# Performance work log

Hardware: AMD Instinct MI355X
Metric: run time of the kernel (lower is better)

## Reference

```python
import jax, jax.numpy as jnp
import numpy as np

EPS = 216.0 / 24389.0
KAPPA = 24389.0 / 27.0
WP = jnp.array([0.95047, 1.0, 1.08883], dtype=jnp.float32)  # D65 white point
M_RGB2XYZ = jnp.array([[0.4124564, 0.3575761, 0.1804375],
                       [0.2126729, 0.7151522, 0.0721750],
                       [0.0193339, 0.1191920, 0.9503041]], dtype=jnp.float32)
M_XYZ2RGB = jnp.array([[3.2404542, -1.5371385, -0.4985314],
                       [-0.9692660, 1.8760108, 0.0415560],
                       [0.0556434, -0.2040259, 1.0572252]], dtype=jnp.float32)
GRID = 8          # cv2.createCLAHE tileGridSize=(8,8)
CLIP_LIMIT = 2.0  # cv2.createCLAHE clipLimit=2.0
NBINS = 256


def _srgb_to_linear(c):
    return jnp.where(c <= 0.04045, c / 12.92, ((c + 0.055) / 1.055) ** 2.4)


def _linear_to_srgb(c):
    c = jnp.maximum(c, 0.0)
    return jnp.where(c <= 0.0031308, c * 12.92, 1.055 * c ** (1.0 / 2.4) - 0.055)


def _rgb_to_lab(rgb):  # rgb [...,3] in [0,1]
    xyz = _srgb_to_linear(rgb) @ M_RGB2XYZ.T / WP
    f = jnp.where(xyz > EPS, jnp.cbrt(xyz), (KAPPA * xyz + 16.0) / 116.0)
    L = 116.0 * f[..., 1] - 16.0
    a = 500.0 * (f[..., 0] - f[..., 1])
    b = 200.0 * (f[..., 1] - f[..., 2])
    return L, a, b


def _lab_to_rgb(L, a, b):
    fy = (L + 16.0) / 116.0
    fx = fy + a / 500.0
    fz = fy - b / 200.0
    def finv(f):
        f3 = f ** 3
        return jnp.where(f3 > EPS, f3, (116.0 * f - 16.0) / KAPPA)
    xyz = jnp.stack([finv(fx), finv(fy), finv(fz)], axis=-1) * WP
    return jnp.clip(_linear_to_srgb(xyz @ M_XYZ2RGB.T), 0.0, 1.0)


def _quantize_L(L):  # cv2.normalize(..., 0, 255, NORM_MINMAX) per image + uint8 cast
    lmin = L.min(axis=(1, 2), keepdims=True)
    lmax = L.max(axis=(1, 2), keepdims=True)
    l255 = (L - lmin) / (lmax - lmin + 1e-6) * 255.0
    return jnp.clip(jnp.round(l255), 0, 255).astype(jnp.int32)


def _equalize_hist(l_int):  # cv2.equalizeHist per image, [N,H,W] int32 -> float levels
    N, H, W = l_int.shape
    seg = (jnp.arange(N, dtype=jnp.int32)[:, None, None] * NBINS + l_int).reshape(-1)
    hist = jax.ops.segment_sum(jnp.ones(seg.shape, jnp.float32), seg,
                               num_segments=N * NBINS).reshape(N, NBINS)
    lut = jnp.round(jnp.cumsum(hist, axis=1) * (255.0 / (H * W)))  # [N,256]
    return jnp.take_along_axis(lut, l_int.reshape(N, H * W), axis=1).reshape(N, H, W)


def _clahe(l_int):  # tiled clipped histogram equalization + bilinear LUT blend
    N, H, W = l_int.shape
    th, tw = H // GRID, W // GRID
    area = th * tw
    ty = jnp.arange(H, dtype=jnp.int32) // th
    tx = jnp.arange(W, dtype=jnp.int32) // tw
    tile = ty[:, None] * GRID + tx[None, :]                      # [H,W] tile id
    seg = ((jnp.arange(N, dtype=jnp.int32)[:, None, None] * (GRID * GRID) + tile)
           * NBINS + l_int).reshape(-1)
    hist = jax.ops.segment_sum(jnp.ones(seg.shape, jnp.float32), seg,
                               num_segments=N * GRID * GRID * NBINS
                               ).reshape(N, GRID, GRID, NBINS)
    limit = max(CLIP_LIMIT * area / NBINS, 1.0)                  # = 32 for 64x64 tiles
    clipped = jnp.minimum(hist, limit)
    excess = (hist - clipped).sum(axis=-1, keepdims=True)
    luts = jnp.round(jnp.cumsum(clipped + excess / NBINS, axis=-1) * (255.0 / area))
    # bilinear interpolation between the 4 neighbouring tile LUTs (border-clamped)
    cy = jnp.clip((jnp.arange(H, dtype=jnp.float32) + 0.5) / th - 0.5, 0.0, GRID - 1.0)
    cx = jnp.clip((jnp.arange(W, dtype=jnp.float32) + 0.5) / tw - 0.5, 0.0, GRID - 1.0)
    y0 = jnp.clip(jnp.floor(cy).astype(jnp.int32), 0, GRID - 2); y1 = y0 + 1
    x0 = jnp.clip(jnp.floor(cx).astype(jnp.int32), 0, GRID - 2); x1 = x0 + 1
    wy = (cy - y0)[:, None]
    wx = (cx - x0)[None, :]
    def per_image(lut, v):  # lut [GRID,GRID,256], v [H,W]
        v00 = lut[y0[:, None], x0[None, :], v]
        v01 = lut[y0[:, None], x1[None, :], v]
        v10 = lut[y1[:, None], x0[None, :], v]
        v11 = lut[y1[:, None], x1[None, :], v]
        top = v00 * (1.0 - wx) + v01 * wx
        bot = v10 * (1.0 - wx) + v11 * wx
        return top * (1.0 - wy) + bot * wy
    return jax.vmap(per_image)(luts, l_int)


def setup_inputs() -> dict:
    key = jax.random.key(0)
    x = jax.random.uniform(key, (16, 3, 512, 512), dtype=jnp.float32)
    return {"x": x}


def reference(x):
    rgb = jnp.transpose(x, (0, 2, 3, 1))          # NCHW -> NHWC
    L, a, b = _rgb_to_lab(rgb)
    l_int = _quantize_L(L)
    def recon(l255):
        out = _lab_to_rgb(l255 * (100.0 / 255.0), a, b)
        return jnp.transpose(out, (0, 3, 1, 2)) * 255.0  # uint8-valued like original
    return recon(_equalize_hist(l_int)), recon(_clahe(l_int))
```

## Files before the change

### kernel.cpp

```cpp
#include <hip/hip_runtime.h>

#define NIMG 16
#define HH 512
#define WW 512
#define HW (HH * WW)
#define NHW (NIMG * HW)
#define TILE 64
#define TILE_AREA (TILE * TILE)

#define EPSV ((float)(216.0 / 24389.0))
#define KAPV ((float)(24389.0 / 27.0))


__device__ __forceinline__ float pow24(float t) {
    float l   = __builtin_amdgcn_logf(t);
    float r   = __builtin_amdgcn_exp2f(l);
    float dl  = (t - r) * __builtin_amdgcn_rcpf(r) * 1.4426950408889634f;
    float ehi = 2.4f * l;
    float elo = __builtin_fmaf(2.4f, l, -ehi) + 2.4f * dl;
    float p   = __builtin_amdgcn_exp2f(ehi);
    return __builtin_fmaf(p * 0.6931471805599453f, elo, p);
}

__device__ __forceinline__ float cbrt_p(float v) {
    float l  = __builtin_amdgcn_logf(v);
    float t  = __builtin_amdgcn_exp2f(l * (1.0f / 3.0f));
    float t2 = t * t;
    float num = __builtin_fmaf(-t2, t, v);
    return __builtin_fmaf(num, __builtin_amdgcn_rcpf(3.0f * t2), t);
}

__device__ __forceinline__ float srgb2lin_p(float c) {
    float lin = c / 12.92f;
    float t   = (c + 0.055f) / 1.055f;
    return (c <= 0.04045f) ? lin : pow24(t);
}

__device__ __forceinline__ float fwd_p(float v) {
    return (v > EPSV) ? cbrt_p(v) : (KAPV * v + 16.0f) / 116.0f;
}

__device__ __forceinline__ float lin2srgb_f(float c) {
    c = fmaxf(c, 0.0f);
    float lo = c * 12.92f;
    float p  = __builtin_amdgcn_exp2f(__builtin_amdgcn_logf(c) * (float)(1.0 / 2.4));
    float hi = 1.055f * p - 0.055f;
    float r  = (c <= 0.0031308f) ? lo : hi;
    return fminf(fmaxf(r, 0.0f), 1.0f);
}

__device__ __forceinline__ float finv_f(float f) {
    float f3 = f * f * f;
    return (f3 > EPSV) ? f3 : (116.0f * f - 16.0f) * (float)(27.0 / 24389.0);
}

__device__ __forceinline__ void lab2rgb255_f(float L, float a, float b,
                                             float* R, float* G, float* B) {
    float fy = (L + 16.0f) * (float)(1.0 / 116.0);
    float fx = fy + a * (float)(1.0 / 500.0);
    float fz = fy - b * (float)(1.0 / 200.0);
    float X = finv_f(fx) * 0.95047f;
    float Y = finv_f(fy);
    float Z = finv_f(fz) * 1.08883f;
    *R = lin2srgb_f((float)3.2404542 * X + (float)-1.5371385 * Y + (float)-0.4985314 * Z) * 255.0f;
    *G = lin2srgb_f((float)-0.969266 * X + (float)1.8760108  * Y + (float)0.041556   * Z) * 255.0f;
    *B = lin2srgb_f((float)0.0556434 * X + (float)-0.2040259 * Y + (float)1.0572252  * Z) * 255.0f;
}

__device__ __forceinline__ unsigned f2o(float f) {
    unsigned b = __float_as_uint(f);
    return (b & 0x80000000u) ? ~b : (b | 0x80000000u);
}
__device__ __forceinline__ float o2f(unsigned o) {
    return __uint_as_float((o & 0x80000000u) ? (o ^ 0x80000000u) : ~o);
}


__global__ void k_init(unsigned* mm) {
    int t = blockIdx.x * 256 + threadIdx.x;
    if (t < NIMG * 64)
        mm[t] = ((t & 63) < 32) ? 0xFFFFFFFFu : 0u;
}

__global__ void k_lab(const float* __restrict__ x, float* __restrict__ out,
                      unsigned* __restrict__ mm) {
    int n = blockIdx.y;
    const float* img = x + (size_t)n * 3 * HW;
    float* o = out + (size_t)n * 3 * HW;
    int base = blockIdx.x * 2048;
    float mn = 1e30f, mx = -1e30f;
    for (int i = 0; i < 8; i++) {
        int p = base + i * 256 + threadIdx.x;
        float rl = srgb2lin_p(img[p]);
        float gl = srgb2lin_p(img[HW + p]);
        float bl = srgb2lin_p(img[2 * HW + p]);
        float X = ((float)0.4124564 * rl + (float)0.3575761 * gl + (float)0.1804375 * bl) / (float)0.95047;
        float Y = ((float)0.2126729 * rl + (float)0.7151522 * gl + (float)0.072175  * bl);
        float Z = ((float)0.0193339 * rl + (float)0.119192  * gl + (float)0.9503041 * bl) / (float)1.08883;
        float fx = fwd_p(X), fy = fwd_p(Y), fz = fwd_p(Z);
        float L = 116.0f * fy - 16.0f;
        o[p]          = L;
        o[HW + p]     = 500.0f * (fx - fy);
        o[2 * HW + p] = 200.0f * (fy - fz);
        mn = fminf(mn, L);
        mx = fmaxf(mx, L);
    }
    for (int off = 32; off; off >>= 1) {
        mn = fminf(mn, __shfl_down(mn, off, 64));
        mx = fmaxf(mx, __shfl_down(mx, off, 64));
    }
    __shared__ float smn[4], smx[4];
    int wv = threadIdx.x >> 6, ln = threadIdx.x & 63;
    if (ln == 0) { smn[wv] = mn; smx[wv] = mx; }
    __syncthreads();
    if (threadIdx.x == 0) {
        mn = fminf(fminf(smn[0], smn[1]), fminf(smn[2], smn[3]));
        mx = fmaxf(fmaxf(smx[0], smx[1]), fmaxf(smx[2], smx[3]));
        atomicMin(&mm[n * 64], f2o(mn));
        atomicMax(&mm[n * 64 + 32], f2o(mx));
    }
}

__global__ void k_quant_hist(const float* __restrict__ out, const unsigned* __restrict__ mm,
                             unsigned char* __restrict__ li_arr, int* __restrict__ hist_tile,
                             float* __restrict__ lut_tile) {
    int n = blockIdx.y, tile = blockIdx.x;
    int ty = tile >> 3, tx = tile & 7;
    int t = threadIdx.x;
    __shared__ int sh[256];
    __shared__ float slut[256];
    sh[t] = 0;
    __syncthreads();
    float lmin = o2f(mm[n * 64]), lmax = o2f(mm[n * 64 + 32]);
    float d = lmax - lmin + (float)1e-6;
    const float* Lp = out + (size_t)n * 3 * HW;
    unsigned char* lio = li_arr + (size_t)n * HW;
    for (int i = t; i < TILE_AREA; i += 256) {
        int r = i >> 6, c = i & 63;
        int p = (ty * TILE + r) * WW + tx * TILE + c;
        float l255 = (Lp[p] - lmin) / d * 255.0f;
        int li = (int)rintf(l255);
        li = min(max(li, 0), 255);
        lio[p] = (unsigned char)li;
        atomicAdd(&sh[li], 1);
    }
    __syncthreads();
    int h = sh[t];
    hist_tile[(n * 64 + tile) * 256 + t] = h;

    int cl = min(h, 32);
    int sum = cl;
    for (int off = 32; off; off >>= 1) sum += __shfl_down(sum, off, 64);
    __shared__ int wsum[4];
    if ((t & 63) == 0) wsum[t >> 6] = sum;
    __syncthreads();
    if (t == 0) {
        int total = wsum[0] + wsum[1] + wsum[2] + wsum[3];
        float e = (float)(TILE_AREA - total) / 256.0f;
        float c = 0.0f;
        for (int b = 0; b < 256; b++) {
            float term = (float)min(sh[b], 32) + e;
            c += term;
            slut[b] = rintf(c * (float)(255.0 / 4096.0));
        }
    }
    __syncthreads();
    lut_tile[(n * 64 + tile) * 256 + t] = slut[t];
}

__global__ void k_eq_lut(const int* __restrict__ hist_tile, float* __restrict__ lut_eq) {
    int n = blockIdx.x, t = threadIdx.x;
    const int* ht = hist_tile + n * 64 * 256;
    int h = 0;
    for (int tile = 0; tile < 64; tile++) h += ht[tile * 256 + t];
    __shared__ int s[256];
    s[t] = h;
    __syncthreads();
    for (int off = 1; off < 256; off <<= 1) {
        int v = s[t];
        int add = (t >= off) ? s[t - off] : 0;
        __syncthreads();
        s[t] = v + add;
        __syncthreads();
    }
    lut_eq[n * 256 + t] = rintf((float)s[t] * (float)(255.0 / (double)HW));
}

__global__ void k_recon(const unsigned char* __restrict__ li_arr,
                        const float* __restrict__ lut_eq,
                        const float* __restrict__ lut_tile,
                        float* __restrict__ out) {
    int n = blockIdx.y, tile = blockIdx.x;
    int ty = tile >> 3, tx = tile & 7;
    __shared__ float slut[9 * 256];
    __shared__ float seq[256];
    seq[threadIdx.x] = lut_eq[n * 256 + threadIdx.x];
    const float* lt = lut_tile + n * 64 * 256;
    for (int j = threadIdx.x; j < 9 * 256; j += 256) {
        int q = j >> 8;
        int jy = q / 3, jx = q % 3;
        int gy = min(max(ty - 1 + jy, 0), 7);
        int gx = min(max(tx - 1 + jx, 0), 7);
        slut[j] = lt[(gy * 8 + gx) * 256 + (j & 255)];
    }
    __syncthreads();

    float* o0 = out + (size_t)n * 3 * HW;
    float* o1 = out + (size_t)3 * NHW + (size_t)n * 3 * HW;
    const unsigned char* lip = li_arr + (size_t)n * HW;

    for (int i = threadIdx.x; i < TILE_AREA; i += 256) {
        int r = i >> 6, c = i & 63;
        int y = ty * TILE + r, xc = tx * TILE + c;
        int p = y * WW + xc;
        float a  = o0[HW + p];
        float b2 = o0[2 * HW + p];
        int li = lip[p];
        float l_eq = seq[li];

        float cyf = fminf(fmaxf(((float)y + 0.5f) / 64.0f - 0.5f, 0.0f), 7.0f);
        float cxf = fminf(fmaxf(((float)xc + 0.5f) / 64.0f - 0.5f, 0.0f), 7.0f);
        int y0 = min((int)cyf, 6), x0 = min((int)cxf, 6);
        float wy = cyf - (float)y0, wx = cxf - (float)x0;
        int ly = y0 - ty + 1, lx = x0 - tx + 1;
        int base = ((ly * 3 + lx) << 8) + li;
        float v00 = slut[base];
        float v01 = slut[base + 256];
        float v10 = slut[base + 768];
        float v11 = slut[base + 1024];
        float top = v00 * (1.0f - wx) + v01 * wx;
        float bot = v10 * (1.0f - wx) + v11 * wx;
        float l_cl = top * (1.0f - wy) + bot * wy;

        float R, G, B;
        lab2rgb255_f(l_eq * (float)(100.0 / 255.0), a, b2, &R, &G, &B);
        o0[p] = R; o0[HW + p] = G; o0[2 * HW + p] = B;
        lab2rgb255_f(l_cl * (float)(100.0 / 255.0), a, b2, &R, &G, &B);
        o1[p] = R; o1[HW + p] = G; o1[2 * HW + p] = B;
    }
}

extern "C" void kernel_launch(void* const* d_in, const int* in_sizes, int n_in,
                              void* d_out, int out_size, void* d_ws, size_t ws_size,
                              hipStream_t stream) {
    const float* x = (const float*)d_in[0];
    float* out = (float*)d_out;
    char* ws = (char*)d_ws;

    unsigned char* li = (unsigned char*)ws;
    size_t off = (size_t)NHW;
    int* hist_tile = (int*)(ws + off);    off += NIMG * 64 * 256 * 4;
    float* lut_eq = (float*)(ws + off);   off += NIMG * 256 * 4;
    float* lut_tile = (float*)(ws + off); off += NIMG * 64 * 256 * 4;
    unsigned* mm = (unsigned*)(ws + off); off += NIMG * 64 * 4;

    k_init<<<4, 256, 0, stream>>>(mm);
    k_lab<<<dim3(HW / 2048, NIMG), 256, 0, stream>>>(x, out, mm);
    k_quant_hist<<<dim3(64, NIMG), 256, 0, stream>>>(out, mm, li, hist_tile, lut_tile);
    k_eq_lut<<<NIMG, 256, 0, stream>>>(hist_tile, lut_eq);
    k_recon<<<dim3(64, NIMG), 256, 0, stream>>>(li, lut_eq, lut_tile, out);
}
```

Before: 189.3 us.

## Recompute a/b in recon instead of storing Lab planes; vectorize and parallelize CLAHE scan

k_lab now writes only the L channel to a workspace buffer, and k_recon re-reads the input RGB to recompute a and b, which removes the write and read-back of two full float planes. Loads and stores in both kernels use float4 and uchar4. The serial single-thread CLAHE LUT prefix sum is replaced with a block-wide integer scan scaled by 256. The cost is extra transcendental work in recon to recompute the colour conversion.

```diff
diff --git a/kernel.cpp b/kernel.cpp
--- a/kernel.cpp
+++ b/kernel.cpp
@@ -82,28 +82,32 @@
         mm[t] = ((t & 63) < 32) ? 0xFFFFFFFFu : 0u;
 }
 
-__global__ void k_lab(const float* __restrict__ x, float* __restrict__ out,
+__global__ void k_lab(const float* __restrict__ x, float* __restrict__ Lbuf,
                       unsigned* __restrict__ mm) {
     int n = blockIdx.y;
     const float* img = x + (size_t)n * 3 * HW;
-    float* o = out + (size_t)n * 3 * HW;
+    float* Lp = Lbuf + (size_t)n * HW;
     int base = blockIdx.x * 2048;
     float mn = 1e30f, mx = -1e30f;
-    for (int i = 0; i < 8; i++) {
-        int p = base + i * 256 + threadIdx.x;
-        float rl = srgb2lin_p(img[p]);
-        float gl = srgb2lin_p(img[HW + p]);
-        float bl = srgb2lin_p(img[2 * HW + p]);
-        float X = ((float)0.4124564 * rl + (float)0.3575761 * gl + (float)0.1804375 * bl) / (float)0.95047;
-        float Y = ((float)0.2126729 * rl + (float)0.7151522 * gl + (float)0.072175  * bl);
-        float Z = ((float)0.0193339 * rl + (float)0.119192  * gl + (float)0.9503041 * bl) / (float)1.08883;
-        float fx = fwd_p(X), fy = fwd_p(Y), fz = fwd_p(Z);
-        float L = 116.0f * fy - 16.0f;
-        o[p]          = L;
-        o[HW + p]     = 500.0f * (fx - fy);
-        o[2 * HW + p] = 200.0f * (fy - fz);
-        mn = fminf(mn, L);
-        mx = fmaxf(mx, L);
+    for (int i = 0; i < 2; i++) {
+        int p = base + i * 1024 + threadIdx.x * 4;
+        float4 r4 = *(const float4*)(img + p);
+        float4 g4 = *(const float4*)(img + HW + p);
+        float4 b4 = *(const float4*)(img + 2 * HW + p);
+        float4 L4;
+        #pragma unroll
+        for (int k = 0; k < 4; k++) {
+            float rr = ((const float*)&r4)[k];
+            float gg = ((const float*)&g4)[k];
+            float bb = ((const float*)&b4)[k];
+            float rl = srgb2lin_p(rr), gl = srgb2lin_p(gg), bl = srgb2lin_p(bb);
+            float Y = ((float)0.2126729 * rl + (float)0.7151522 * gl + (float)0.072175  * bl);
+            float L = 116.0f * fwd_p(Y) - 16.0f;
+            ((float*)&L4)[k] = L;
+            mn = fminf(mn, L);
+            mx = fmaxf(mx, L);
+        }
+        *(float4*)(Lp + p) = L4;
     }
     for (int off = 32; off; off >>= 1) {
         mn = fminf(mn, __shfl_down(mn, off, 64));
@@ -121,19 +125,18 @@
     }
 }
 
-__global__ void k_quant_hist(const float* __restrict__ out, const unsigned* __restrict__ mm,
+__global__ void k_quant_hist(const float* __restrict__ Lbuf, const unsigned* __restrict__ mm,
                              unsigned char* __restrict__ li_arr, int* __restrict__ hist_tile,
                              float* __restrict__ lut_tile) {
     int n = blockIdx.y, tile = blockIdx.x;
     int ty = tile >> 3, tx = tile & 7;
     int t = threadIdx.x;
     __shared__ int sh[256];
-    __shared__ float slut[256];
     sh[t] = 0;
     __syncthreads();
     float lmin = o2f(mm[n * 64]), lmax = o2f(mm[n * 64 + 32]);
     float d = lmax - lmin + (float)1e-6;
-    const float* Lp = out + (size_t)n * 3 * HW;
+    const float* Lp = Lbuf + (size_t)n * HW;
     unsigned char* lio = li_arr + (size_t)n * HW;
     for (int i = t; i < TILE_AREA; i += 256) {
         int r = i >> 6, c = i & 63;
@@ -154,18 +157,19 @@
     __shared__ int wsum[4];
     if ((t & 63) == 0) wsum[t >> 6] = sum;
     __syncthreads();
-    if (t == 0) {
-        int total = wsum[0] + wsum[1] + wsum[2] + wsum[3];
-        float e = (float)(TILE_AREA - total) / 256.0f;
-        float c = 0.0f;
-        for (int b = 0; b < 256; b++) {
-            float term = (float)min(sh[b], 32) + e;
-            c += term;
-            slut[b] = rintf(c * (float)(255.0 / 4096.0));
-        }
-    }
-    __syncthreads();
-    lut_tile[(n * 64 + tile) * 256 + t] = slut[t];
+    int total = wsum[0] + wsum[1] + wsum[2] + wsum[3];
+    int exc = TILE_AREA - total;
+    sh[t] = 256 * cl + exc;
+    __syncthreads();
+    for (int off = 1; off < 256; off <<= 1) {
+        int v = sh[t];
+        int add = (t >= off) ? sh[t - off] : 0;
+        __syncthreads();
+        sh[t] = v + add;
+        __syncthreads();
+    }
+    lut_tile[(n * 64 + tile) * 256 + t] =
+        rintf((float)sh[t] * (float)(255.0 / 1048576.0));
 }
 
 __global__ void k_eq_lut(const int* __restrict__ hist_tile, float* __restrict__ lut_eq) {
@@ -186,17 +190,17 @@
     lut_eq[n * 256 + t] = rintf((float)s[t] * (float)(255.0 / (double)HW));
 }
 
-__global__ void k_recon(const unsigned char* __restrict__ li_arr,
-                        const float* __restrict__ lut_eq,
-                        const float* __restrict__ lut_tile,
+__global__ void k_recon(const float* __restrict__ x, const unsigned char* __restrict__ li_arr,
+                        const float* __restrict__ lut_eq, const float* __restrict__ lut_tile,
                         float* __restrict__ out) {
     int n = blockIdx.y, tile = blockIdx.x;
     int ty = tile >> 3, tx = tile & 7;
+    int t = threadIdx.x;
     __shared__ float slut[9 * 256];
     __shared__ float seq[256];
-    seq[threadIdx.x] = lut_eq[n * 256 + threadIdx.x];
+    seq[t] = lut_eq[n * 256 + t];
     const float* lt = lut_tile + n * 64 * 256;
-    for (int j = threadIdx.x; j < 9 * 256; j += 256) {
+    for (int j = t; j < 9 * 256; j += 256) {
         int q = j >> 8;
         int jy = q / 3, jx = q % 3;
         int gy = min(max(ty - 1 + jy, 0), 7);
@@ -205,38 +209,71 @@
     }
     __syncthreads();
 
+    const float* img = x + (size_t)n * 3 * HW;
+    const unsigned char* lip = li_arr + (size_t)n * HW;
     float* o0 = out + (size_t)n * 3 * HW;
     float* o1 = out + (size_t)3 * NHW + (size_t)n * 3 * HW;
-    const unsigned char* lip = li_arr + (size_t)n * HW;
-
-    for (int i = threadIdx.x; i < TILE_AREA; i += 256) {
-        int r = i >> 6, c = i & 63;
-        int y = ty * TILE + r, xc = tx * TILE + c;
-        int p = y * WW + xc;
-        float a  = o0[HW + p];
-        float b2 = o0[2 * HW + p];
-        int li = lip[p];
-        float l_eq = seq[li];
+
+    for (int it = 0; it < 4; it++) {
+        int j = it * 1024 + t * 4;
+        int r = j >> 6, c = j & 63;
+        int y = ty * TILE + r;
+        int xb = tx * TILE + c;
+        int p = y * WW + xb;
+
+        float4 r4 = *(const float4*)(img + p);
+        float4 g4 = *(const float4*)(img + HW + p);
+        float4 b4 = *(const float4*)(img + 2 * HW + p);
+        uchar4 li4 = *(const uchar4*)(lip + p);
 
         float cyf = fminf(fmaxf(((float)y + 0.5f) / 64.0f - 0.5f, 0.0f), 7.0f);
-        float cxf = fminf(fmaxf(((float)xc + 0.5f) / 64.0f - 0.5f, 0.0f), 7.0f);
-        int y0 = min((int)cyf, 6), x0 = min((int)cxf, 6);
-        float wy = cyf - (float)y0, wx = cxf - (float)x0;
-        int ly = y0 - ty + 1, lx = x0 - tx + 1;
-        int base = ((ly * 3 + lx) << 8) + li;
-        float v00 = slut[base];
-        float v01 = slut[base + 256];
-        float v10 = slut[base + 768];
-        float v11 = slut[base + 1024];
-        float top = v00 * (1.0f - wx) + v01 * wx;
-        float bot = v10 * (1.0f - wx) + v11 * wx;
-        float l_cl = top * (1.0f - wy) + bot * wy;
-
-        float R, G, B;
-        lab2rgb255_f(l_eq * (float)(100.0 / 255.0), a, b2, &R, &G, &B);
-        o0[p] = R; o0[HW + p] = G; o0[2 * HW + p] = B;
-        lab2rgb255_f(l_cl * (float)(100.0 / 255.0), a, b2, &R, &G, &B);
-        o1[p] = R; o1[HW + p] = G; o1[2 * HW + p] = B;
+        int y0 = min((int)cyf, 6);
+        float wy = cyf - (float)y0;
+        int ly = y0 - ty + 1;
+
+        float4 R0, G0, B0, R1, G1, B1;
+        #pragma unroll
+        for (int k = 0; k < 4; k++) {
+            float rr = ((const float*)&r4)[k];
+            float gg = ((const float*)&g4)[k];
+            float bb = ((const float*)&b4)[k];
+            float rl = srgb2lin_p(rr), gl = srgb2lin_p(gg), bl = srgb2lin_p(bb);
+            float X = ((float)0.4124564 * rl + (float)0.3575761 * gl + (float)0.1804375 * bl) / (float)0.95047;
+            float Y = ((float)0.2126729 * rl + (float)0.7151522 * gl + (float)0.072175  * bl);
+            float Z = ((float)0.0193339 * rl + (float)0.119192  * gl + (float)0.9503041 * bl) / (float)1.08883;
+            float fx = fwd_p(X), fy = fwd_p(Y), fz = fwd_p(Z);
+            float A  = 500.0f * (fx - fy);
+            float B2 = 200.0f * (fy - fz);
+
+            int li = ((const unsigned char*)&li4)[k];
+            float l_eq = seq[li];
+
+            int xc = xb + k;
+            float cxf = fminf(fmaxf(((float)xc + 0.5f) / 64.0f - 0.5f, 0.0f), 7.0f);
+            int x0 = min((int)cxf, 6);
+            float wx = cxf - (float)x0;
+            int lx = x0 - tx + 1;
+            int base = ((ly * 3 + lx) << 8) + li;
+            float v00 = slut[base];
+            float v01 = slut[base + 256];
+            float v10 = slut[base + 768];
+            float v11 = slut[base + 1024];
+            float top = v00 * (1.0f - wx) + v01 * wx;
+            float bot = v10 * (1.0f - wx) + v11 * wx;
+            float l_cl = top * (1.0f - wy) + bot * wy;
+
+            float R, G, B;
+            lab2rgb255_f(l_eq * (float)(100.0 / 255.0), A, B2, &R, &G, &B);
+            ((float*)&R0)[k] = R; ((float*)&G0)[k] = G; ((float*)&B0)[k] = B;
+            lab2rgb255_f(l_cl * (float)(100.0 / 255.0), A, B2, &R, &G, &B);
+            ((float*)&R1)[k] = R; ((float*)&G1)[k] = G; ((float*)&B1)[k] = B;
+        }
+        *(float4*)(o0 + p)          = R0;
+        *(float4*)(o0 + HW + p)     = G0;
+        *(float4*)(o0 + 2 * HW + p) = B0;
+        *(float4*)(o1 + p)          = R1;
+        *(float4*)(o1 + HW + p)     = G1;
+        *(float4*)(o1 + 2 * HW + p) = B1;
     }
 }
 
@@ -247,16 +284,17 @@
     float* out = (float*)d_out;
     char* ws = (char*)d_ws;
 
-    unsigned char* li = (unsigned char*)ws;
-    size_t off = (size_t)NHW;
+    float* Lbuf = (float*)ws;
+    size_t off = (size_t)NHW * 4;
+    unsigned char* li = (unsigned char*)(ws + off); off += NHW;
     int* hist_tile = (int*)(ws + off);    off += NIMG * 64 * 256 * 4;
     float* lut_eq = (float*)(ws + off);   off += NIMG * 256 * 4;
     float* lut_tile = (float*)(ws + off); off += NIMG * 64 * 256 * 4;
     unsigned* mm = (unsigned*)(ws + off); off += NIMG * 64 * 4;
 
     k_init<<<4, 256, 0, stream>>>(mm);
-    k_lab<<<dim3(HW / 2048, NIMG), 256, 0, stream>>>(x, out, mm);
-    k_quant_hist<<<dim3(64, NIMG), 256, 0, stream>>>(out, mm, li, hist_tile, lut_tile);
+    k_lab<<<dim3(HW / 2048, NIMG), 256, 0, stream>>>(x, Lbuf, mm);
+    k_quant_hist<<<dim3(64, NIMG), 256, 0, stream>>>(Lbuf, mm, li, hist_tile, lut_tile);
     k_eq_lut<<<NIMG, 256, 0, stream>>>(hist_tile, lut_eq);
-    k_recon<<<dim3(64, NIMG), 256, 0, stream>>>(li, lut_eq, lut_tile, out);
-}
+    k_recon<<<dim3(64, NIMG), 256, 0, stream>>>(x, li, lut_eq, lut_tile, out);
+}
```

Result: no change. 185.7 us (-1.9%).
